# Optimization experiments

Measured on AMD Instinct MI355X. Metric: run time of the kernel, lower is better.

The kernel has to match this reference:

```python
import jax, jax.numpy as jnp
import numpy as np


def qdq(x):
    """Per-tensor symmetric int8 quantize-dequantize (act_quant + fp8_gemm dequant semantics)."""
    scale = jnp.maximum(jnp.max(jnp.abs(x)) / 127.0, 1e-8)
    q = jnp.clip(jnp.round(x / scale), -127.0, 127.0) * scale
    # straight-through estimator so the reference is also usable under autodiff
    return x + jax.lax.stop_gradient(q - x)


def layernorm(x, scale, bias, eps=1e-6):
    mean = jnp.mean(x, axis=-1, keepdims=True)
    var = jnp.mean(jnp.square(x - mean), axis=-1, keepdims=True)
    return (x - mean) * jax.lax.rsqrt(var + eps) * scale + bias


def glin(t, W, b):
    """TPUGEMMLinear: quantized GEMM (dequantized matmul) + bias."""
    return jnp.matmul(qdq(t), qdq(W)) + b


def setup_inputs() -> dict:
    key = jax.random.key(0)
    ks = jax.random.split(key, 12)
    B, S, D = 4, 1024, 1024
    H, HD, F, P = 32, 32, 4096, 32
    lecun = lambda k, shape: jax.random.normal(k, shape, jnp.float32) * (1.0 / np.sqrt(shape[0]))
    return {
        'inputs': jax.random.normal(ks[0], (B, S, D), jnp.float32),
        'ln1_scale': jnp.ones((D,), jnp.float32),
        'ln1_bias': jnp.zeros((D,), jnp.float32),
        'Wq': lecun(ks[1], (D, H * HD)), 'bq': jnp.zeros((H * HD,), jnp.float32),
        'Wk': lecun(ks[2], (D, H * HD)), 'bk': jnp.zeros((H * HD,), jnp.float32),
        'Wv': lecun(ks[3], (D, H * HD)), 'bv': jnp.zeros((H * HD,), jnp.float32),
        'rel_pos_emb': jax.random.normal(ks[4], (2 * P + 1, HD), jnp.float32) * 0.02,
        'Wo': lecun(ks[5], (H * HD, D)), 'bo': jnp.zeros((D,), jnp.float32),
        'ln2_scale': jnp.ones((D,), jnp.float32),
        'ln2_bias': jnp.zeros((D,), jnp.float32),
        'W1': lecun(ks[6], (D, F)), 'b1': jnp.zeros((F,), jnp.float32),
        'W2': lecun(ks[7], (F, D)), 'b2': jnp.zeros((D,), jnp.float32),
    }


def reference(inputs, ln1_scale, ln1_bias, Wq, bq, Wk, bk, Wv, bv, rel_pos_emb,
              Wo, bo, ln2_scale, ln2_bias, W1, b1, W2, b2):
    B, S, D = inputs.shape
    HD = rel_pos_emb.shape[1]
    H = D // HD
    P = (rel_pos_emb.shape[0] - 1) // 2

    # Pre-attention LayerNorm (TPULayerNorm, eps=1e-6)
    x = layernorm(inputs, ln1_scale, ln1_bias)

    # Quantized QKV projections
    q = glin(x, Wq, bq).reshape(B, S, H, HD).transpose(0, 2, 1, 3)  # [B,H,S,HD]
    k = glin(x, Wk, bk).reshape(B, S, H, HD).transpose(0, 2, 1, 3)
    v = glin(x, Wv, bv).reshape(B, S, H, HD).transpose(0, 2, 1, 3)

    # Relative position bias: [1, HD, S, S] broadcast onto head axis (HD == H by construction)
    pos = jnp.clip(jnp.arange(S)[:, None] - jnp.arange(S)[None, :] + P, 0, 2 * P)
    rel_bias = rel_pos_emb[pos].transpose(2, 0, 1)[None]  # [1, HD, S, S]

    # Quantized content scores + bias, custom scale factor
    scores = jnp.einsum('bhqd,bhkd->bhqk', qdq(q), qdq(k)) + rel_bias
    scale = jnp.sqrt(jnp.asarray(HD, jnp.float32)) * jnp.power(jnp.asarray(S, jnp.float32), 0.25)
    scores = scores / scale

    # Stable softmax with +1e-6 denominator (as in source)
    m = jnp.max(scores, axis=-1, keepdims=True)
    e = jnp.exp(scores - m)
    w = e / (jnp.sum(e, axis=-1, keepdims=True) + 1e-6)

    attn = jnp.einsum('bhqk,bhkd->bhqd', w, qdq(v))  # values quantized, weights not
    attn = attn.transpose(0, 2, 1, 3).reshape(B, S, H * HD)
    attn_out = glin(attn, Wo, bo)

    xr = attn_out + inputs
    y = layernorm(xr, ln2_scale, ln2_bias)

    # MLP (_mlp_tpu assumed: quantized Linear -> gelu -> quantized Linear)
    h = jax.nn.gelu(glin(y, W1, b1))
    out = glin(h, W2, b2)
    # NOTE: source returns mlp_output directly (no second residual add)
    return out
```

## Files before the change

### kernel.cpp

```cpp
#include <hip/hip_runtime.h>
#include <cstdint>


typedef unsigned short u16;
typedef __bf16 bf16x4 __attribute__((ext_vector_type(4)));
typedef __bf16 bf16x8 __attribute__((ext_vector_type(8)));
typedef float  f32x4  __attribute__((ext_vector_type(4)));

#define MFMA(a, b, c) __builtin_amdgcn_mfma_f32_16x16x32_bf16(a, b, c, 0, 0, 0)

#define NSLOT 13
#define PSPREAD 64
#define PSTRIDE 16
#define SLOTSZ (PSPREAD * PSTRIDE)

__device__ __forceinline__ float bf2f(u16 h) {
    return __uint_as_float(((unsigned)h) << 16);
}
__device__ __forceinline__ u16 f2bf(float f) {
    unsigned u = __float_as_uint(f);
    u += 0x7FFFu + ((u >> 16) & 1u);
    return (u16)(u >> 16);
}
__device__ __forceinline__ float qdqv(float v, float s) {
    float q = rintf(v / s);
    q = fminf(fmaxf(q, -127.f), 127.f);
    return q * s;
}

__device__ __forceinline__ float getscale64(const int* scales, int slot) {
    float m = __int_as_float(scales[slot * SLOTSZ + (threadIdx.x & 63) * PSTRIDE]);
#pragma unroll
    for (int o = 32; o > 0; o >>= 1) m = fmaxf(m, __shfl_xor(m, o));
    return fmaxf(m / 127.f, 1e-8f);
}

typedef const __attribute__((address_space(1))) unsigned gas_u32;
typedef __attribute__((address_space(3))) unsigned las_u32;
__device__ __forceinline__ void gld16(const void* g, void* l) {
    __builtin_amdgcn_global_load_lds((gas_u32*)g, (las_u32*)l, 16, 0, 0);
}

__global__ void zero_k(int* s) {
    const int i = blockIdx.x * 256 + threadIdx.x;
    if (i < NSLOT * SLOTSZ) s[i] = 0;
}

__device__ __forceinline__ float blk_sum(float v, float* red) {
#pragma unroll
    for (int o = 32; o > 0; o >>= 1) v += __shfl_xor(v, o);
    __syncthreads();
    if ((threadIdx.x & 63) == 0) red[threadIdx.x >> 6] = v;
    __syncthreads();
    return red[0] + red[1] + red[2] + red[3];
}

__device__ __forceinline__ void blk_absmax_commit(float am, float* red, int* scales,
                                                  int slot, int bidx) {
#pragma unroll
    for (int o = 32; o > 0; o >>= 1) am = fmaxf(am, __shfl_xor(am, o));
    __syncthreads();
    if ((threadIdx.x & 63) == 0) red[threadIdx.x >> 6] = am;
    __syncthreads();
    if (threadIdx.x == 0) {
        float m = fmaxf(fmaxf(red[0], red[1]), fmaxf(red[2], red[3]));
        atomicMax(scales + slot * SLOTSZ + ((bidx & (PSPREAD - 1)) * PSTRIDE),
                  __float_as_int(m));
    }
}

__global__ __launch_bounds__(256) void waln_k(const float* __restrict__ w0, const float* __restrict__ w1,
                                              const float* __restrict__ w2, const float* __restrict__ w3,
                                              const float* __restrict__ w4, const float* __restrict__ w5,
                                              const float* __restrict__ in, const float* __restrict__ gam,
                                              const float* __restrict__ bet, u16* __restrict__ out,
                                              int* __restrict__ scales) {
    __shared__ float red[4];
    const int tid = threadIdx.x;
    if (blockIdx.x < 3072) {
        const int b = blockIdx.x;
        int ti, boff;
        if (b < 1024)      { ti = b >> 8; boff = (b & 255) * 4096; }
        else if (b < 2048) { ti = 4;      boff = (b - 1024) * 4096; }
        else               { ti = 5;      boff = (b - 2048) * 4096; }
        const float* w = (ti == 0) ? w0 : (ti == 1) ? w1 : (ti == 2) ? w2
                       : (ti == 3) ? w3 : (ti == 4) ? w4 : w5;
        const float4* wv = (const float4*)(w + boff);
        float m = 0.f;
#pragma unroll
        for (int k = 0; k < 4; k++) {
            float4 v = wv[tid + k * 256];
            m = fmaxf(m, fmaxf(fmaxf(fabsf(v.x), fabsf(v.y)), fmaxf(fabsf(v.z), fabsf(v.w))));
        }
#pragma unroll
        for (int o = 32; o > 0; o >>= 1) m = fmaxf(m, __shfl_xor(m, o));
        if ((tid & 63) == 0)
            atomicMax(scales + (7 + ti) * SLOTSZ + (((b * 4 + (tid >> 6)) & (PSPREAD - 1)) * PSTRIDE),
                      __float_as_int(m));
        return;
    }
    const long row = blockIdx.x - 3072;
    float4 v = ((const float4*)(in + row * 1024))[tid];
    float mean = blk_sum(v.x + v.y + v.z + v.w, red) * (1.f / 1024.f);
    float dx = v.x - mean, dy = v.y - mean, dz = v.z - mean, dw = v.w - mean;
    float var = blk_sum(dx * dx + dy * dy + dz * dz + dw * dw, red) * (1.f / 1024.f);
    float inv = rsqrtf(var + 1e-6f);
    float4 gg = ((const float4*)gam)[tid];
    float4 bb = ((const float4*)bet)[tid];
    float o0 = dx * inv * gg.x + bb.x, o1 = dy * inv * gg.y + bb.y;
    float o2 = dz * inv * gg.z + bb.z, o3 = dw * inv * gg.w + bb.w;
    ushort4 st;
    st.x = f2bf(o0); st.y = f2bf(o1); st.z = f2bf(o2); st.w = f2bf(o3);
    ((ushort4*)(out + row * 1024))[tid] = st;
    float am = fmaxf(fmaxf(fabsf(o0), fabsf(o1)), fmaxf(fabsf(o2), fabsf(o3)));
    blk_absmax_commit(am, red, scales, 0, (int)row);
}

__global__ __launch_bounds__(256) void wqt6_k(const float* __restrict__ w0, const float* __restrict__ w1,
                                              const float* __restrict__ w2, const float* __restrict__ w3,
                                              const float* __restrict__ w4, const float* __restrict__ w5,
                                              u16* __restrict__ wtbase, const int* __restrict__ scales) {
    __shared__ float t[32][33];
    const int b = blockIdx.x;
    const float* W;
    u16* Wt;
    int K, N, bx, by, slot;
    if (b < 4096) {
        const int ti = b >> 10, r = b & 1023;
        W = (ti == 0) ? w0 : (ti == 1) ? w1 : (ti == 2) ? w2 : w3;
        Wt = wtbase + (long)ti * 1048576;
        K = 1024; N = 1024; bx = r & 31; by = r >> 5; slot = 7 + ti;
    } else if (b < 8192) {
        const int r = b - 4096;
        W = w4; Wt = wtbase + 4194304;
        K = 1024; N = 4096; bx = r & 127; by = r >> 7; slot = 11;
    } else {
        const int r = b - 8192;
        W = w5; Wt = wtbase + 8388608;
        K = 4096; N = 1024; bx = r & 31; by = r >> 5; slot = 12;
    }
    const int n0 = bx * 32, k0 = by * 32;
    const float s = getscale64(scales, slot);
    const int c = threadIdx.x & 31, r0 = threadIdx.x >> 5;
#pragma unroll
    for (int i = 0; i < 4; i++) {
        int kk = k0 + r0 + i * 8;
        t[r0 + i * 8][c] = qdqv(W[(long)kk * N + n0 + c], s);
    }
    __syncthreads();
#pragma unroll
    for (int i = 0; i < 4; i++) {
        int nn = n0 + r0 + i * 8;
        Wt[(long)nn * K + k0 + c] = f2bf(t[c][r0 + i * 8]);
    }
}

__global__ __launch_bounds__(256) void ln2comb_k(const float* __restrict__ p, const float* __restrict__ bo,
                                                 const float* __restrict__ inputs,
                                                 const float* __restrict__ gam, const float* __restrict__ bet,
                                                 u16* __restrict__ out, int* __restrict__ scales) {
    __shared__ float red[4];
    const long row = blockIdx.x;
    const int tid = threadIdx.x;
    float4 a = ((const float4*)(p + row * 1024))[tid];
    float4 b = ((const float4*)(p + 4194304 + row * 1024))[tid];
    float4 bb0 = ((const float4*)bo)[tid];
    float4 xi = ((const float4*)(inputs + row * 1024))[tid];
    float4 v;
    v.x = a.x + b.x + bb0.x + xi.x; v.y = a.y + b.y + bb0.y + xi.y;
    v.z = a.z + b.z + bb0.z + xi.z; v.w = a.w + b.w + bb0.w + xi.w;
    float mean = blk_sum(v.x + v.y + v.z + v.w, red) * (1.f / 1024.f);
    float dx = v.x - mean, dy = v.y - mean, dz = v.z - mean, dw = v.w - mean;
    float var = blk_sum(dx * dx + dy * dy + dz * dz + dw * dw, red) * (1.f / 1024.f);
    float inv = rsqrtf(var + 1e-6f);
    float4 gg = ((const float4*)gam)[tid];
    float4 bb = ((const float4*)bet)[tid];
    float o0 = dx * inv * gg.x + bb.x, o1 = dy * inv * gg.y + bb.y;
    float o2 = dz * inv * gg.z + bb.z, o3 = dw * inv * gg.w + bb.w;
    ushort4 st;
    st.x = f2bf(o0); st.y = f2bf(o1); st.z = f2bf(o2); st.w = f2bf(o3);
    ((ushort4*)(out + row * 1024))[tid] = st;
    float am = fmaxf(fmaxf(fabsf(o0), fabsf(o1)), fmaxf(fabsf(o2), fabsf(o3)));
    blk_absmax_commit(am, red, scales, 5, (int)row);
}

__global__ void combo_k(const float* __restrict__ pa, const float* __restrict__ pc,
                        const float* __restrict__ b2, float* __restrict__ out) {
    const int i = blockIdx.x * 256 + threadIdx.x;
    float4 a0 = ((const float4*)pa)[i];
    float4 a1 = ((const float4*)(pa + 4194304))[i];
    float4 c0 = ((const float4*)pc)[i];
    float4 c1 = ((const float4*)out)[i];
    float4 bb = ((const float4*)b2)[i & 255];
    float4 o;
    o.x = ((a0.x + a1.x) + (c0.x + c1.x)) + bb.x;
    o.y = ((a0.y + a1.y) + (c0.y + c1.y)) + bb.y;
    o.z = ((a0.z + a1.z) + (c0.z + c1.z)) + bb.z;
    o.w = ((a0.w + a1.w) + (c0.w + c1.w)) + bb.w;
    ((float4*)out)[i] = o;
}

__global__ void qact_k(u16* buf, int n8, const int* __restrict__ scales, int slot) {
    const float s = getscale64(scales, slot);
    int i = blockIdx.x * 256 + threadIdx.x;
    if (i >= n8) return;
    uint4 u = ((const uint4*)buf)[i];
    unsigned w[4] = {u.x, u.y, u.z, u.w};
#pragma unroll
    for (int j = 0; j < 4; j++) {
        float lo = qdqv(bf2f((u16)(w[j] & 0xFFFFu)), s);
        float hi = qdqv(bf2f((u16)(w[j] >> 16)), s);
        w[j] = (unsigned)f2bf(lo) | ((unsigned)f2bf(hi) << 16);
    }
    uint4 o; o.x = w[0]; o.y = w[1]; o.z = w[2]; o.w = w[3];
    ((uint4*)buf)[i] = o;
}

__global__ __launch_bounds__(256) void vq_k(u16* __restrict__ qk, const u16* __restrict__ v,
                                            u16* __restrict__ vt, const int* __restrict__ scales) {
    __shared__ u16 t[32][33];
    const int tid = threadIdx.x;
    if (blockIdx.x < 4096) {
        const int i = blockIdx.x * 256 + tid;
        const int slot = (i >= 524288) ? 2 : 1;
        const float s = getscale64(scales, slot);
        uint4 u = ((const uint4*)qk)[i];
        unsigned w[4] = {u.x, u.y, u.z, u.w};
#pragma unroll
        for (int j = 0; j < 4; j++) {
            float lo = qdqv(bf2f((u16)(w[j] & 0xFFFFu)), s);
            float hi = qdqv(bf2f((u16)(w[j] >> 16)), s);
            w[j] = (unsigned)f2bf(lo) | ((unsigned)f2bf(hi) << 16);
        }
        uint4 o; o.x = w[0]; o.y = w[1]; o.z = w[2]; o.w = w[3];
        ((uint4*)qk)[i] = o;
        return;
    }
    const int r = blockIdx.x - 4096;
    const int bh = r >> 5, s0 = (r & 31) * 32;
    const float s = getscale64(scales, 3);
    const int c = tid & 31, r0 = tid >> 5;
    const u16* src = v + ((long)bh * 1024 + s0) * 32;
#pragma unroll
    for (int i = 0; i < 4; i++) {
        int rr = r0 + i * 8;
        t[rr][c] = f2bf(qdqv(bf2f(src[rr * 32 + c]), s));
    }
    __syncthreads();
    u16* dst = vt + (long)bh * 32768;
#pragma unroll
    for (int i = 0; i < 4; i++) {
        int rr = r0 + i * 8;
        dst[(long)rr * 1024 + s0 + c] = t[c][rr];
    }
}

template <int EPI>
__global__ __launch_bounds__(256, 2) void gemm_k(const u16* __restrict__ A, const u16* __restrict__ Bt,
                                                 const float* __restrict__ bias, const float* __restrict__ bias2,
                                                 const float* __restrict__ bias3,
                                                 int M, int N, int Kfull, int Kslice,
                                                 float* __restrict__ outf, float* __restrict__ outf2,
                                                 float* __restrict__ outf3, u16* __restrict__ outb,
                                                 int* __restrict__ scales, int slot) {
    __shared__ u16 As[128 * 64];
    __shared__ u16 Bs[128 * 64];
    const float* bp = bias;
    long koff = 0, ooff = 0;
    float* po = outf;
    if (EPI == 0) {
        const int z = blockIdx.z;
        Bt += (long)z * 1048576;
        outb += (long)z * 4194304;
        bp = (z == 0) ? bias : (z == 1 ? bias2 : bias3);
        slot += z;
    }
    if (EPI == 4) {
        const int z = blockIdx.z;
        koff = (long)z * Kslice * 2;
        if (z < 2)       { po = outf;  ooff = (long)z * M * N; }
        else if (z == 2) { po = outf2; ooff = 0; }
        else             { po = outf3; ooff = 0; }
    }
    const int tid = threadIdx.x;
    const int lane = tid & 63;
    const int wave = tid >> 6;
    const int wm = wave >> 1, wn = wave & 1;
    const int bm = blockIdx.y * 128, bn = blockIdx.x * 128;
    const int g = lane >> 4, c = lane & 15;

    const long astride = (long)Kfull * 2;
    const int srow = wave * 32 + (lane >> 3);
    const int scol = ((lane & 7) * 16) ^ ((lane >> 3) << 4);
    const char* Ag = (const char*)A + (long)(bm + srow) * astride + scol + koff;
    const char* Bg = (const char*)Bt + (long)(bn + srow) * astride + scol + koff;
    char* Al = (char*)As + wave * 4096;
    char* Bl = (char*)Bs + wave * 4096;

    f32x4 acc[4][4];
    const f32x4 zf = {0.f, 0.f, 0.f, 0.f};
#pragma unroll
    for (int i = 0; i < 4; i++)
#pragma unroll
        for (int j = 0; j < 4; j++) acc[i][j] = zf;

    const int nk = Kslice >> 6;
    for (int kt = 0; kt < nk; ++kt) {
        __syncthreads();
        const long ko = (long)kt * 128;
#pragma unroll
        for (int i = 0; i < 4; i++) gld16(Ag + ko + (long)(i * 8) * astride, Al + i * 1024);
#pragma unroll
        for (int i = 0; i < 4; i++) gld16(Bg + ko + (long)(i * 8) * astride, Bl + i * 1024);
        __syncthreads();

#pragma unroll
        for (int kh = 0; kh < 2; kh++) {
            bf16x8 af[4], bq[4];
            const int kb = kh * 64 + g * 16;
            const int sw = kb ^ ((c & 7) << 4);
#pragma unroll
            for (int i = 0; i < 4; i++)
                af[i] = *(const bf16x8*)((const char*)As + (wm * 64 + i * 16 + c) * 128 + sw);
#pragma unroll
            for (int j = 0; j < 4; j++)
                bq[j] = *(const bf16x8*)((const char*)Bs + (wn * 64 + j * 16 + c) * 128 + sw);
#pragma unroll
            for (int i = 0; i < 4; i++)
#pragma unroll
                for (int j = 0; j < 4; j++)
                    acc[i][j] = MFMA(af[i], bq[j], acc[i][j]);
        }
    }

    float am = 0.f;
#pragma unroll
    for (int i = 0; i < 4; i++) {
#pragma unroll
        for (int j = 0; j < 4; j++) {
#pragma unroll
            for (int t = 0; t < 4; t++) {
                const int row = bm + wm * 64 + i * 16 + g * 4 + t;
                const int col = bn + wn * 64 + j * 16 + c;
                if (EPI == 0) {
                    float v = acc[i][j][t] + bp[col];
                    long oi = ((long)((row >> 10) * 32 + (col >> 5))) * 32768
                              + (long)(row & 1023) * 32 + (col & 31);
                    outb[oi] = f2bf(v);
                    am = fmaxf(am, fabsf(v));
                } else if (EPI == 2) {
                    float v = acc[i][j][t] + bp[col];
                    float t3 = v * v * v;
                    float gl = 0.5f * v * (1.f + tanhf(0.79788456080286536f * (v + 0.044715f * t3)));
                    outb[(long)row * N + col] = f2bf(gl);
                    am = fmaxf(am, fabsf(gl));
                } else {
                    po[ooff + (long)row * N + col] = acc[i][j][t];
                }
            }
        }
    }
    if (EPI == 0 || EPI == 2) {
#pragma unroll
        for (int o = 32; o > 0; o >>= 1) am = fmaxf(am, __shfl_xor(am, o));
        if (lane == 0)
            atomicMax(scales + slot * SLOTSZ
                          + ((((blockIdx.x + blockIdx.y * gridDim.x) * 4 + wave) & (PSPREAD - 1)) * PSTRIDE),
                      __float_as_int(am));
    }
}

__global__ __launch_bounds__(256, 8) void attn_k(const u16* __restrict__ q, const u16* __restrict__ k,
                                                 const u16* __restrict__ vt, const float* __restrict__ relpos,
                                                 u16* __restrict__ attn, int* __restrict__ scales) {
    __shared__ float rel_s[65];
    __shared__ __align__(16) u16 P[4][16 * 40];
    __shared__ float frs[4][16];
    const int tid = threadIdx.x;
    const int lane = tid & 63;
    const int w = tid >> 6;
    const int bh = blockIdx.x;
    const int b = bh >> 5, h = bh & 31;
    const int q0 = (blockIdx.y * 4 + w) * 16;
    const int g = lane >> 4, c = lane & 15;
    const float SC = 0.03125f;
    for (int i = tid; i < 65; i += 256) rel_s[i] = relpos[i * 32 + h] * SC;
    __syncthreads();
    const float rb0 = rel_s[0], rb64 = rel_s[64];

    const u16* qb = q + ((long)bh * 1024 + q0) * 32;
    const u16* kb = k + (long)bh * 32768;
    const u16* vb = vt + (long)bh * 32768;
    u16* Pw = P[w];
    float* fw = frs[w];

    bf16x8 aq = *(const bf16x8*)(qb + c * 32 + g * 8);

    const f32x4 zf = {0.f, 0.f, 0.f, 0.f};
    f32x4 o0 = zf, o1 = zf;
    float m_run = -1e30f, l_run = 0.f;

    for (int kt = 0; kt < 32; ++kt) {
        const int kk = kt * 32;
        bf16x8 bk0 = *(const bf16x8*)(kb + (kk + c) * 32 + g * 8);
        bf16x8 bk1 = *(const bf16x8*)(kb + (kk + 16 + c) * 32 + g * 8);
        bf16x8 bv0 = *(const bf16x8*)(vb + c * 1024 + kk + g * 8);
        bf16x8 bv1 = *(const bf16x8*)(vb + (16 + c) * 1024 + kk + g * 8);
        const int mode = (kk >= q0 + 48) ? 0 : (kk <= q0 - 64) ? 1 : 2;

        f32x4 s0 = MFMA(bk0, aq, zf);
        f32x4 s1 = MFMA(bk1, aq, zf);
        float v[8];
        if (mode == 0) {
#pragma unroll
            for (int t = 0; t < 4; t++) { v[t] = fmaf(s0[t], SC, rb0); v[4 + t] = fmaf(s1[t], SC, rb0); }
        } else if (mode == 1) {
#pragma unroll
            for (int t = 0; t < 4; t++) { v[t] = fmaf(s0[t], SC, rb64); v[4 + t] = fmaf(s1[t], SC, rb64); }
        } else {
            const int base = (q0 + c) - kk - g * 4 + 32;
#pragma unroll
            for (int t = 0; t < 4; t++) {
                int d0 = min(max(base - t, 0), 64);
                int d1 = min(max(base - 16 - t, 0), 64);
                v[t] = fmaf(s0[t], SC, rel_s[d0]);
                v[4 + t] = fmaf(s1[t], SC, rel_s[d1]);
            }
        }
        float mt = fmaxf(fmaxf(fmaxf(v[0], v[1]), fmaxf(v[2], v[3])),
                         fmaxf(fmaxf(v[4], v[5]), fmaxf(v[6], v[7])));
        mt = fmaxf(mt, __shfl_xor(mt, 16));
        mt = fmaxf(mt, __shfl_xor(mt, 32));
        const float mn = fmaxf(m_run, mt);
        const float fr = __expf(m_run - mn);
        float sm = 0.f;
        bf16x4 pk0, pk1;
#pragma unroll
        for (int t = 0; t < 4; t++) {
            float p = __expf(v[t] - mn);     sm += p; pk0[t] = (__bf16)p;
            float p2 = __expf(v[4 + t] - mn); sm += p2; pk1[t] = (__bf16)p2;
        }
        sm += __shfl_xor(sm, 16);
        sm += __shfl_xor(sm, 32);
        l_run = l_run * fr + sm;
        m_run = mn;
        *(bf16x4*)&Pw[c * 40 + g * 4] = pk0;
        *(bf16x4*)&Pw[c * 40 + 16 + g * 4] = pk1;

        if (__any(fr != 1.f)) {
            if (g == 0) fw[c] = fr;
            float4 f0 = *(float4*)&fw[g * 4];
            o0[0] *= f0.x; o0[1] *= f0.y; o0[2] *= f0.z; o0[3] *= f0.w;
            o1[0] *= f0.x; o1[1] *= f0.y; o1[2] *= f0.z; o1[3] *= f0.w;
        }
        bf16x8 ap = *(const bf16x8*)&Pw[c * 40 + g * 8];
        o0 = MFMA(ap, bv0, o0);
        o1 = MFMA(ap, bv1, o1);
    }

    if (g == 0) fw[c] = l_run;
    float4 l0 = *(float4*)&fw[g * 4];
    float lv[4] = {l0.x, l0.y, l0.z, l0.w};
    float am = 0.f;
#pragma unroll
    for (int t = 0; t < 4; t++) {
        const long row = (long)b * 1024 + q0 + g * 4 + t;
        float v0 = o0[t] / (lv[t] + 1e-6f);
        float v1 = o1[t] / (lv[t] + 1e-6f);
        attn[row * 1024 + h * 32 + c] = f2bf(v0);
        attn[row * 1024 + h * 32 + 16 + c] = f2bf(v1);
        am = fmaxf(am, fmaxf(fabsf(v0), fabsf(v1)));
    }
#pragma unroll
    for (int o2 = 32; o2 > 0; o2 >>= 1) am = fmaxf(am, __shfl_xor(am, o2));
    if (lane == 0)
        atomicMax(scales + 4 * SLOTSZ + ((((bh * 16 + blockIdx.y) * 4 + w) & (PSPREAD - 1)) * PSTRIDE),
                  __float_as_int(am));
}

extern "C" void kernel_launch(void* const* d_in, const int* in_sizes, int n_in,
                              void* d_out, int out_size, void* d_ws, size_t ws_size,
                              hipStream_t stream) {
    (void)in_sizes; (void)n_in; (void)out_size; (void)ws_size;
    const float* inputs = (const float*)d_in[0];
    const float* ln1s   = (const float*)d_in[1];
    const float* ln1b   = (const float*)d_in[2];
    const float* Wq     = (const float*)d_in[3];
    const float* bq     = (const float*)d_in[4];
    const float* Wk     = (const float*)d_in[5];
    const float* bk     = (const float*)d_in[6];
    const float* Wv     = (const float*)d_in[7];
    const float* bv     = (const float*)d_in[8];
    const float* rel    = (const float*)d_in[9];
    const float* Wo     = (const float*)d_in[10];
    const float* bo     = (const float*)d_in[11];
    const float* ln2s   = (const float*)d_in[12];
    const float* ln2b   = (const float*)d_in[13];
    const float* W1     = (const float*)d_in[14];
    const float* b1     = (const float*)d_in[15];
    const float* W2     = (const float*)d_in[16];
    const float* b2     = (const float*)d_in[17];
    float* out = (float*)d_out;

    char* ws = (char*)d_ws;
    int* scales = (int*)ws;
    char* regionA = ws + 65536;
    char* regionB = regionA + (32u << 20);
    char* regionC = regionB + (32u << 20);
    u16* qb    = (u16*)regionA;
    u16* kbuf  = qb + 4194304;
    u16* vbuf  = kbuf + 4194304;
    u16* vtb   = vbuf + 4194304;
    float* pWo = (float*)regionA;
    u16* hb    = (u16*)regionA;
    u16* xq    = (u16*)regionB;
    u16* attnb = xq;
    u16* yb    = xq + 4194304;
    float* pW2  = (float*)regionB;
    float* pW2c = (float*)regionC;
    u16* wtb   = (u16*)regionC;

    zero_k<<<52, 256, 0, stream>>>(scales);
    waln_k<<<7168, 256, 0, stream>>>(Wq, Wk, Wv, Wo, W1, W2, inputs, ln1s, ln1b, xq, scales);

    wqt6_k<<<12288, 256, 0, stream>>>(Wq, Wk, Wv, Wo, W1, W2, wtb, scales);

    qact_k<<<2048, 256, 0, stream>>>(xq, 524288, scales, 0);

    gemm_k<0><<<dim3(8, 32, 3), 256, 0, stream>>>(xq, wtb, bq, bk, bv, 4096, 1024, 1024, 1024,
                                                  nullptr, nullptr, nullptr, qb, scales, 1);

    vq_k<<<8192, 256, 0, stream>>>(qb, vbuf, vtb, scales);

    attn_k<<<dim3(128, 16), 256, 0, stream>>>(qb, kbuf, vtb, rel, attnb, scales);
    qact_k<<<2048, 256, 0, stream>>>(attnb, 524288, scales, 4);

    gemm_k<4><<<dim3(8, 32, 2), 256, 0, stream>>>(attnb, wtb + 3145728, nullptr, nullptr, nullptr,
                                                  4096, 1024, 1024, 512, pWo, nullptr, nullptr, nullptr,
                                                  scales, -1);
    ln2comb_k<<<4096, 256, 0, stream>>>(pWo, bo, inputs, ln2s, ln2b, yb, scales);
    qact_k<<<2048, 256, 0, stream>>>(yb, 524288, scales, 5);

    gemm_k<2><<<dim3(32, 32), 256, 0, stream>>>(yb, wtb + 4194304, b1, nullptr, nullptr,
                                                4096, 4096, 1024, 1024, nullptr, nullptr, nullptr, hb,
                                                scales, 6);
    qact_k<<<8192, 256, 0, stream>>>(hb, 2097152, scales, 6);

    gemm_k<4><<<dim3(8, 32, 4), 256, 0, stream>>>(hb, wtb + 8388608, nullptr, nullptr, nullptr,
                                                  4096, 1024, 4096, 1024, pW2, pW2c, out, nullptr,
                                                  scales, -1);
    combo_k<<<4096, 256, 0, stream>>>(pW2, pW2c, b2, out);
}
```

Before: 345.2 us.

## Process 32 query rows per wave in attention and prefetch next K/V tile

Each wave in the attention kernel now handles two 16-row query tiles, so every K and V fragment loaded from global memory feeds twice the MFMA work, and the grid is halved. The K/V loads for the next key tile are issued before the current tile's compute as a software prefetch. The mode boundary is widened to cover 32 rows, and the launch-bounds occupancy hint is dropped. In exchange the kernel holds more registers and uses more shared memory per block, which can lower occupancy and leave fewer blocks to spread across the GPU.

```diff
diff --git a/kernel.cpp b/kernel.cpp
--- a/kernel.cpp
+++ b/kernel.cpp
@@ -370,18 +370,18 @@
     }
 }
 
-__global__ __launch_bounds__(256, 8) void attn_k(const u16* __restrict__ q, const u16* __restrict__ k,
-                                                 const u16* __restrict__ vt, const float* __restrict__ relpos,
-                                                 u16* __restrict__ attn, int* __restrict__ scales) {
+__global__ __launch_bounds__(256) void attn_k(const u16* __restrict__ q, const u16* __restrict__ k,
+                                              const u16* __restrict__ vt, const float* __restrict__ relpos,
+                                              u16* __restrict__ attn, int* __restrict__ scales) {
     __shared__ float rel_s[65];
-    __shared__ __align__(16) u16 P[4][16 * 40];
-    __shared__ float frs[4][16];
+    __shared__ __align__(16) u16 P[4][32 * 40];
+    __shared__ float frs[4][32];
     const int tid = threadIdx.x;
     const int lane = tid & 63;
     const int w = tid >> 6;
     const int bh = blockIdx.x;
     const int b = bh >> 5, h = bh & 31;
-    const int q0 = (blockIdx.y * 4 + w) * 16;
+    const int q0 = blockIdx.y * 128 + w * 32;
     const int g = lane >> 4, c = lane & 15;
     const float SC = 0.03125f;
     for (int i = tid; i < 65; i += 256) rel_s[i] = relpos[i * 32 + h] * SC;
@@ -394,87 +394,111 @@
     u16* Pw = P[w];
     float* fw = frs[w];
 
-    bf16x8 aq = *(const bf16x8*)(qb + c * 32 + g * 8);
+    bf16x8 aq[2];
+#pragma unroll
+    for (int i = 0; i < 2; i++) aq[i] = *(const bf16x8*)(qb + (i * 16 + c) * 32 + g * 8);
 
     const f32x4 zf = {0.f, 0.f, 0.f, 0.f};
-    f32x4 o0 = zf, o1 = zf;
-    float m_run = -1e30f, l_run = 0.f;
+    f32x4 o[2][2] = {{zf, zf}, {zf, zf}};
+    float m_run[2] = {-1e30f, -1e30f};
+    float l_run[2] = {0.f, 0.f};
+
+    bf16x8 bk0 = *(const bf16x8*)(kb + (0 + c) * 32 + g * 8);
+    bf16x8 bk1 = *(const bf16x8*)(kb + (16 + c) * 32 + g * 8);
+    bf16x8 bv0 = *(const bf16x8*)(vb + c * 1024 + 0 + g * 8);
+    bf16x8 bv1 = *(const bf16x8*)(vb + (16 + c) * 1024 + 0 + g * 8);
 
     for (int kt = 0; kt < 32; ++kt) {
         const int kk = kt * 32;
-        bf16x8 bk0 = *(const bf16x8*)(kb + (kk + c) * 32 + g * 8);
-        bf16x8 bk1 = *(const bf16x8*)(kb + (kk + 16 + c) * 32 + g * 8);
-        bf16x8 bv0 = *(const bf16x8*)(vb + c * 1024 + kk + g * 8);
-        bf16x8 bv1 = *(const bf16x8*)(vb + (16 + c) * 1024 + kk + g * 8);
-        const int mode = (kk >= q0 + 48) ? 0 : (kk <= q0 - 64) ? 1 : 2;
-
-        f32x4 s0 = MFMA(bk0, aq, zf);
-        f32x4 s1 = MFMA(bk1, aq, zf);
-        float v[8];
-        if (mode == 0) {
-#pragma unroll
-            for (int t = 0; t < 4; t++) { v[t] = fmaf(s0[t], SC, rb0); v[4 + t] = fmaf(s1[t], SC, rb0); }
-        } else if (mode == 1) {
-#pragma unroll
-            for (int t = 0; t < 4; t++) { v[t] = fmaf(s0[t], SC, rb64); v[4 + t] = fmaf(s1[t], SC, rb64); }
-        } else {
-            const int base = (q0 + c) - kk - g * 4 + 32;
+        const int kkn = ((kt + 1) & 31) * 32;
+        bf16x8 nk0 = *(const bf16x8*)(kb + (kkn + c) * 32 + g * 8);
+        bf16x8 nk1 = *(const bf16x8*)(kb + (kkn + 16 + c) * 32 + g * 8);
+        bf16x8 nv0 = *(const bf16x8*)(vb + c * 1024 + kkn + g * 8);
+        bf16x8 nv1 = *(const bf16x8*)(vb + (16 + c) * 1024 + kkn + g * 8);
+
+        const int mode = (kk >= q0 + 64) ? 0 : (kk <= q0 - 64) ? 1 : 2;
+        float frv[2];
+#pragma unroll
+        for (int i = 0; i < 2; i++) {
+            f32x4 s0 = MFMA(bk0, aq[i], zf);
+            f32x4 s1 = MFMA(bk1, aq[i], zf);
+            float v[8];
+            if (mode == 0) {
+#pragma unroll
+                for (int t = 0; t < 4; t++) { v[t] = fmaf(s0[t], SC, rb0); v[4 + t] = fmaf(s1[t], SC, rb0); }
+            } else if (mode == 1) {
+#pragma unroll
+                for (int t = 0; t < 4; t++) { v[t] = fmaf(s0[t], SC, rb64); v[4 + t] = fmaf(s1[t], SC, rb64); }
+            } else {
+                const int base = (q0 + i * 16 + c) - kk - g * 4 + 32;
+#pragma unroll
+                for (int t = 0; t < 4; t++) {
+                    int d0 = min(max(base - t, 0), 64);
+                    int d1 = min(max(base - 16 - t, 0), 64);
+                    v[t] = fmaf(s0[t], SC, rel_s[d0]);
+                    v[4 + t] = fmaf(s1[t], SC, rel_s[d1]);
+                }
+            }
+            float mt = fmaxf(fmaxf(fmaxf(v[0], v[1]), fmaxf(v[2], v[3])),
+                             fmaxf(fmaxf(v[4], v[5]), fmaxf(v[6], v[7])));
+            mt = fmaxf(mt, __shfl_xor(mt, 16));
+            mt = fmaxf(mt, __shfl_xor(mt, 32));
+            const float mn = fmaxf(m_run[i], mt);
+            const float fr = __expf(m_run[i] - mn);
+            frv[i] = fr;
+            float sm = 0.f;
+            bf16x4 pk0, pk1;
 #pragma unroll
             for (int t = 0; t < 4; t++) {
-                int d0 = min(max(base - t, 0), 64);
-                int d1 = min(max(base - 16 - t, 0), 64);
-                v[t] = fmaf(s0[t], SC, rel_s[d0]);
-                v[4 + t] = fmaf(s1[t], SC, rel_s[d1]);
+                float p = __expf(v[t] - mn);     sm += p; pk0[t] = (__bf16)p;
+                float p2 = __expf(v[4 + t] - mn); sm += p2; pk1[t] = (__bf16)p2;
+            }
+            sm += __shfl_xor(sm, 16);
+            sm += __shfl_xor(sm, 32);
+            l_run[i] = l_run[i] * fr + sm;
+            m_run[i] = mn;
+            *(bf16x4*)&Pw[(i * 16 + c) * 40 + g * 4] = pk0;
+            *(bf16x4*)&Pw[(i * 16 + c) * 40 + 16 + g * 4] = pk1;
+        }
+        if (__any((frv[0] != 1.f) | (frv[1] != 1.f))) {
+            if (g == 0) { fw[c] = frv[0]; fw[16 + c] = frv[1]; }
+            float4 f0 = *(float4*)&fw[g * 4];
+            float4 f1 = *(float4*)&fw[16 + g * 4];
+#pragma unroll
+            for (int j = 0; j < 2; j++) {
+                o[0][j][0] *= f0.x; o[0][j][1] *= f0.y; o[0][j][2] *= f0.z; o[0][j][3] *= f0.w;
+                o[1][j][0] *= f1.x; o[1][j][1] *= f1.y; o[1][j][2] *= f1.z; o[1][j][3] *= f1.w;
             }
         }
-        float mt = fmaxf(fmaxf(fmaxf(v[0], v[1]), fmaxf(v[2], v[3])),
-                         fmaxf(fmaxf(v[4], v[5]), fmaxf(v[6], v[7])));
-        mt = fmaxf(mt, __shfl_xor(mt, 16));
-        mt = fmaxf(mt, __shfl_xor(mt, 32));
-        const float mn = fmaxf(m_run, mt);
-        const float fr = __expf(m_run - mn);
-        float sm = 0.f;
-        bf16x4 pk0, pk1;
-#pragma unroll
-        for (int t = 0; t < 4; t++) {
-            float p = __expf(v[t] - mn);     sm += p; pk0[t] = (__bf16)p;
-            float p2 = __expf(v[4 + t] - mn); sm += p2; pk1[t] = (__bf16)p2;
-        }
-        sm += __shfl_xor(sm, 16);
-        sm += __shfl_xor(sm, 32);
-        l_run = l_run * fr + sm;
-        m_run = mn;
-        *(bf16x4*)&Pw[c * 40 + g * 4] = pk0;
-        *(bf16x4*)&Pw[c * 40 + 16 + g * 4] = pk1;
-
-        if (__any(fr != 1.f)) {
-            if (g == 0) fw[c] = fr;
-            float4 f0 = *(float4*)&fw[g * 4];
-            o0[0] *= f0.x; o0[1] *= f0.y; o0[2] *= f0.z; o0[3] *= f0.w;
-            o1[0] *= f0.x; o1[1] *= f0.y; o1[2] *= f0.z; o1[3] *= f0.w;
-        }
-        bf16x8 ap = *(const bf16x8*)&Pw[c * 40 + g * 8];
-        o0 = MFMA(ap, bv0, o0);
-        o1 = MFMA(ap, bv1, o1);
-    }
-
-    if (g == 0) fw[c] = l_run;
+        bf16x8 ap0 = *(const bf16x8*)&Pw[c * 40 + g * 8];
+        bf16x8 ap1 = *(const bf16x8*)&Pw[(16 + c) * 40 + g * 8];
+        o[0][0] = MFMA(ap0, bv0, o[0][0]);
+        o[0][1] = MFMA(ap0, bv1, o[0][1]);
+        o[1][0] = MFMA(ap1, bv0, o[1][0]);
+        o[1][1] = MFMA(ap1, bv1, o[1][1]);
+        bk0 = nk0; bk1 = nk1; bv0 = nv0; bv1 = nv1;
+    }
+
+    if (g == 0) { fw[c] = l_run[0]; fw[16 + c] = l_run[1]; }
     float4 l0 = *(float4*)&fw[g * 4];
-    float lv[4] = {l0.x, l0.y, l0.z, l0.w};
+    float4 l1 = *(float4*)&fw[16 + g * 4];
+    float lv[2][4] = {{l0.x, l0.y, l0.z, l0.w}, {l1.x, l1.y, l1.z, l1.w}};
     float am = 0.f;
 #pragma unroll
-    for (int t = 0; t < 4; t++) {
-        const long row = (long)b * 1024 + q0 + g * 4 + t;
-        float v0 = o0[t] / (lv[t] + 1e-6f);
-        float v1 = o1[t] / (lv[t] + 1e-6f);
-        attn[row * 1024 + h * 32 + c] = f2bf(v0);
-        attn[row * 1024 + h * 32 + 16 + c] = f2bf(v1);
-        am = fmaxf(am, fmaxf(fabsf(v0), fabsf(v1)));
-    }
+    for (int i = 0; i < 2; i++)
+#pragma unroll
+        for (int j = 0; j < 2; j++)
+#pragma unroll
+            for (int t = 0; t < 4; t++) {
+                float val = o[i][j][t] / (lv[i][t] + 1e-6f);
+                long row = (long)b * 1024 + q0 + i * 16 + g * 4 + t;
+                attn[row * 1024 + h * 32 + j * 16 + c] = f2bf(val);
+                am = fmaxf(am, fabsf(val));
+            }
 #pragma unroll
     for (int o2 = 32; o2 > 0; o2 >>= 1) am = fmaxf(am, __shfl_xor(am, o2));
     if (lane == 0)
-        atomicMax(scales + 4 * SLOTSZ + ((((bh * 16 + blockIdx.y) * 4 + w) & (PSPREAD - 1)) * PSTRIDE),
+        atomicMax(scales + 4 * SLOTSZ + ((((bh * 8 + blockIdx.y) * 4 + w) & (PSPREAD - 1)) * PSTRIDE),
                   __float_as_int(am));
 }
 
@@ -532,7 +556,7 @@
 
     vq_k<<<8192, 256, 0, stream>>>(qb, vbuf, vtb, scales);
 
-    attn_k<<<dim3(128, 16), 256, 0, stream>>>(qb, kbuf, vtb, rel, attnb, scales);
+    attn_k<<<dim3(128, 8), 256, 0, stream>>>(qb, kbuf, vtb, rel, attnb, scales);
     qact_k<<<2048, 256, 0, stream>>>(attnb, 524288, scales, 4);
 
     gemm_k<4><<<dim3(8, 32, 2), 256, 0, stream>>>(attnb, wtb + 3145728, nullptr, nullptr, nullptr,
```

Measured after the change: 323.9 us. 1.07x faster.
